# Kernel tuning notes

Hardware: AMD Instinct MI355X
Metric: run time of the kernel (lower is better)

Reference implementation:

```python
import jax, jax.numpy as jnp
import numpy as np

SRC, B, SNT, E, C, V, EXT = 512, 16, 512, 512, 512, 12000, 500


def setup_inputs() -> dict:
    key = jax.random.key(0)
    ks = jax.random.split(key, 12)
    alignment_weight = jax.random.uniform(ks[0], (SRC, B, SNT), dtype=jnp.float32)
    arc_weight = jax.random.uniform(ks[1], (SRC, B, SRC), dtype=jnp.float32)
    rel_weight = jnp.zeros((1,), jnp.float32)
    concept_outs = jax.random.normal(ks[2], (SRC, B, E), dtype=jnp.float32)
    copy_seq = jax.random.randint(ks[3], (SNT, B, 2), 0, V + EXT)
    # pin the max so tot_ext = V + EXT is deterministic (torch uses copy_seq.max().item())
    copy_seq = copy_seq.at[0, 0, 0].set(V + EXT - 1)
    target = jax.random.randint(ks[4], (SRC, B), 0, V)
    target_rel = jnp.zeros((1,), jnp.int64 if jax.config.read('jax_enable_x64') else jnp.int32)
    std = 0.02
    W_transfer = jax.random.normal(ks[5], (C, E), jnp.float32) * std
    b_transfer = jnp.zeros((C,), jnp.float32)
    W_gen = jax.random.normal(ks[6], (V, C), jnp.float32) * std
    b_gen = jnp.zeros((V,), jnp.float32)
    W_div = jax.random.normal(ks[7], (3, C), jnp.float32) * std
    b_div = jnp.zeros((3,), jnp.float32)
    return dict(alignment_weight=alignment_weight, arc_weight=arc_weight,
                rel_weight=rel_weight, concept_outs=concept_outs,
                copy_seq=copy_seq, target=target, target_rel=target_rel,
                bsz=B, src_len=SRC,
                W_transfer=W_transfer, b_transfer=b_transfer,
                W_gen=W_gen, b_gen=b_gen, W_div=W_div, b_div=b_div)


def reference(alignment_weight, arc_weight, rel_weight, concept_outs, copy_seq,
              target, target_rel, bsz, src_len,
              W_transfer, b_transfer, W_gen, b_gen, W_div, b_div):
    # work=True inference path of ArcConceptDecoder (joint_rel=False, separate_rel=False)
    snt_len = alignment_weight.shape[-1]
    copy_seq = copy_seq[:snt_len]                       # [snt, B, 2]
    h = jnp.tanh(concept_outs @ W_transfer.T + b_transfer)  # [src, B, C]
    gates = jax.nn.softmax(h @ W_div.T + b_div, axis=-1)     # [src, B, 3]
    gen_gate = gates[..., 0:1]
    map_gate = gates[..., 1:2]
    copy_gate = gates[..., 2:3]
    copy_gate2 = jnp.concatenate([copy_gate, map_gate], axis=-1)  # [src, B, 2]
    probs = gen_gate * jax.nn.softmax(h @ W_gen.T + b_gen, axis=-1)  # [src, B, V]
    vocab = probs.shape[-1]
    tot_ext = vocab + EXT
    probs = jnp.concatenate(
        [probs, jnp.zeros(probs.shape[:-1] + (tot_ext - vocab,), probs.dtype)], axis=-1)
    # index: copy_seq.transpose(0,1).view(1,B,-1).expand(src,-1,-1)
    index = jnp.transpose(copy_seq, (1, 0, 2)).reshape(1, probs.shape[1], -1)  # [1, B, snt*2]
    index = jnp.broadcast_to(index, (probs.shape[0],) + index.shape[1:])       # [src, B, snt*2]
    copy_probs = (copy_gate2[:, :, None, :] * alignment_weight[..., None])
    copy_probs = copy_probs.reshape(probs.shape[0], probs.shape[1], -1)        # [src, B, snt*2]
    # scatter_add along last dim
    S, Bv = probs.shape[0], probs.shape[1]
    flat_probs = probs.reshape(S * Bv, tot_ext)
    flat_idx = index.reshape(S * Bv, -1)
    flat_cp = copy_probs.reshape(S * Bv, -1)
    rows = jnp.arange(S * Bv)[:, None]
    flat_probs = flat_probs.at[rows, flat_idx].add(flat_cp)
    probs = flat_probs.reshape(S, Bv, tot_ext)
    ll = jnp.log(probs + 1e-12)
    arc_ll = jnp.log(arc_weight + 1e-12)
    return ll, arc_ll
```

## Files before the change

kernel.cpp:

```cpp
#include <hip/hip_runtime.h>
#include <hip/hip_bf16.h>

#define SRCL 512
#define BSZ  16
#define SNTL 512
#define CDIM 512
#define KDIM 512
#define VOC  12000
#define EXTN 500
#define MROWS (SRCL*BSZ)
#define TOTV (VOC+EXTN)
#define NPAD 12032
#define LL_SIZE ((size_t)MROWS * TOTV)

typedef __attribute__((ext_vector_type(8))) short bf16x8;
typedef __attribute__((ext_vector_type(4))) float f32x4;

__device__ __forceinline__ unsigned short f2bf(float x) {
  union { __hip_bfloat16 b; unsigned short u; } c;
  c.b = __float2bfloat16(x);
  return c.u;
}
__device__ __forceinline__ float bflo(unsigned int u) { return __uint_as_float(u << 16); }
__device__ __forceinline__ float bfhi(unsigned int u) { return __uint_as_float(u & 0xffff0000u); }

__device__ __forceinline__ void gload16(const void* g, void* l) {
  __builtin_amdgcn_global_load_lds(
      (const __attribute__((address_space(1))) unsigned int*)g,
      (__attribute__((address_space(3))) unsigned int*)l, 16, 0, 0);
}

__device__ __forceinline__ float wred_max(float v) {
  for (int o = 32; o; o >>= 1) v = fmaxf(v, __shfl_down(v, o, 64));
  return v;
}
__device__ __forceinline__ float wred_sum(float v) {
  for (int o = 32; o; o >>= 1) v += __shfl_down(v, o, 64);
  return v;
}

__global__ void cvt_kernel(const float* __restrict__ co, const float* __restrict__ wt,
                           const float* __restrict__ wg,
                           unsigned short* __restrict__ cob,
                           unsigned short* __restrict__ wtb,
                           unsigned short* __restrict__ wgb) {
  const int stride = gridDim.x * blockDim.x;
  const int t0 = blockIdx.x * blockDim.x + threadIdx.x;
  for (int i = t0; i < MROWS*KDIM/4; i += stride) {
    const float4 v = ((const float4*)co)[i];
    ushort4 o; o.x = f2bf(v.x); o.y = f2bf(v.y); o.z = f2bf(v.z); o.w = f2bf(v.w);
    ((ushort4*)cob)[i] = o;
  }
  for (int i = t0; i < CDIM*KDIM/4; i += stride) {
    const float4 v = ((const float4*)wt)[i];
    ushort4 o; o.x = f2bf(v.x); o.y = f2bf(v.y); o.z = f2bf(v.z); o.w = f2bf(v.w);
    ((ushort4*)wtb)[i] = o;
  }
  for (int i = t0; i < NPAD*KDIM/4; i += stride) {
    float4 v = make_float4(0.f, 0.f, 0.f, 0.f);
    if (i < VOC*KDIM/4) v = ((const float4*)wg)[i];
    ushort4 o; o.x = f2bf(v.x); o.y = f2bf(v.y); o.z = f2bf(v.z); o.w = f2bf(v.w);
    ((ushort4*)wgb)[i] = o;
  }
}

template<int EPI>
__launch_bounds__(256)
__global__ void gemm_bt(const short* __restrict__ A, const short* __restrict__ Bm,
                        const float* __restrict__ bias, void* __restrict__ outp) {
  __shared__ short As[128*32];
  __shared__ short Bs[128*32];
  const int tid  = threadIdx.x;
  const int wave = tid >> 6;
  const int lane = tid & 63;
  const int m0 = blockIdx.y * 128;
  const int n0 = blockIdx.x * 128;

  const int lrow = lane >> 2;
  const int lkof = (lane & 3) * 8;
  const size_t aG0 = (size_t)(m0 + wave*32 + lrow) * KDIM + lkof;
  const size_t aG1 = aG0 + (size_t)16 * KDIM;
  const size_t bG0 = (size_t)(n0 + wave*32 + lrow) * KDIM + lkof;
  const size_t bG1 = bG0 + (size_t)16 * KDIM;
  short* lA0 = As + wave*1024;  short* lA1 = lA0 + 512;
  short* lB0 = Bs + wave*1024;  short* lB1 = lB0 + 512;

  const int wm = wave & 1, wn = wave >> 1;
  const int quad = lane >> 4, r16 = lane & 15;
  const int aoff = (wm*64 + r16)*32 + quad*8;
  const int boff = (wn*64 + r16)*32 + quad*8;

  f32x4 acc[4][4];
#pragma unroll
  for (int i = 0; i < 4; ++i)
#pragma unroll
    for (int j = 0; j < 4; ++j) acc[i][j] = (f32x4){0.f,0.f,0.f,0.f};

  for (int kt = 0; kt < KDIM/32; ++kt) {
    const int kof = kt * 32;
    __syncthreads();
    gload16(A  + aG0 + kof, lA0);
    gload16(A  + aG1 + kof, lA1);
    gload16(Bm + bG0 + kof, lB0);
    gload16(Bm + bG1 + kof, lB1);
    __syncthreads();
    bf16x8 af[4], bf[4];
#pragma unroll
    for (int i = 0; i < 4; ++i) {
      af[i] = *(const bf16x8*)(As + aoff + i*512);
      bf[i] = *(const bf16x8*)(Bs + boff + i*512);
    }
#pragma unroll
    for (int mi = 0; mi < 4; ++mi)
#pragma unroll
      for (int ni = 0; ni < 4; ++ni)
        acc[mi][ni] = __builtin_amdgcn_mfma_f32_16x16x32_bf16(af[mi], bf[ni], acc[mi][ni], 0, 0, 0);
  }

#pragma unroll
  for (int mi = 0; mi < 4; ++mi) {
#pragma unroll
    for (int ni = 0; ni < 4; ++ni) {
#pragma unroll
      for (int r = 0; r < 4; ++r) {
        const int row = m0 + wm*64 + mi*16 + quad*4 + r;
        const int col = n0 + wn*64 + ni*16 + r16;
        float v = acc[mi][ni][r];
        if constexpr (EPI == 0) {
          v = tanhf(v + bias[col]);
          ((unsigned short*)outp)[(size_t)row * CDIM + col] = f2bf(v);
        } else if constexpr (EPI == 1) {
          v += (col < VOC) ? bias[col] : 0.f;
          ((float*)outp)[(size_t)row * TOTV + col] = v;
        } else {
          v += (col < VOC) ? bias[col] : 0.f;
          ((unsigned short*)outp)[(size_t)row * NPAD + col] = f2bf(v);
        }
      }
    }
  }
}

__launch_bounds__(256)
__global__ void gates_kernel(const __hip_bfloat16* __restrict__ h,
                             const float* __restrict__ Wd, const float* __restrict__ bd,
                             float* __restrict__ gates) {
  __shared__ float scr[12];
  const int m = blockIdx.x;
  float d0 = 0.f, d1 = 0.f, d2 = 0.f;
  for (int c = threadIdx.x; c < CDIM; c += 256) {
    const float hv = __bfloat162float(h[(size_t)m*CDIM + c]);
    d0 += hv * Wd[c];
    d1 += hv * Wd[CDIM + c];
    d2 += hv * Wd[2*CDIM + c];
  }
  d0 = wred_sum(d0); d1 = wred_sum(d1); d2 = wred_sum(d2);
  const int w = threadIdx.x >> 6;
  if ((threadIdx.x & 63) == 0) { scr[w*3] = d0; scr[w*3+1] = d1; scr[w*3+2] = d2; }
  __syncthreads();
  if (threadIdx.x == 0) {
    float g0 = bd[0], g1 = bd[1], g2 = bd[2];
    for (int i = 0; i < 4; ++i) { g0 += scr[i*3]; g1 += scr[i*3+1]; g2 += scr[i*3+2]; }
    const float mx = fmaxf(g0, fmaxf(g1, g2));
    const float e0 = __expf(g0-mx), e1 = __expf(g1-mx), e2 = __expf(g2-mx);
    const float inv = 1.f / (e0 + e1 + e2);
    gates[m*3+0] = e0*inv; gates[m*3+1] = e1*inv; gates[m*3+2] = e2*inv;
  }
}

template<int BF16L>
__launch_bounds__(1024)
__global__ void finalize_kernel(const void* __restrict__ lg, float* __restrict__ out,
                                const float* __restrict__ gates,
                                const int* __restrict__ copy_seq,
                                const float* __restrict__ align) {
  __shared__ __align__(16) float p[TOTV];
  __shared__ float scr[16];
  const int m = blockIdx.x;
  const int b = m & 15;
  const int tid = threadIdx.x;
  float* row = out + (size_t)m * TOTV;

  float mx = -1e30f;
  if constexpr (BF16L) {
    const uint4* rowv = (const uint4*)((const unsigned short*)lg + (size_t)m * NPAD);
    for (int i = tid; i < VOC/8; i += 1024) {
      const uint4 q = rowv[i];
      const float v0 = bflo(q.x), v1 = bfhi(q.x), v2 = bflo(q.y), v3 = bfhi(q.y);
      const float v4 = bflo(q.z), v5 = bfhi(q.z), v6 = bflo(q.w), v7 = bfhi(q.w);
      const int base = i*8;
      p[base+0]=v0; p[base+1]=v1; p[base+2]=v2; p[base+3]=v3;
      p[base+4]=v4; p[base+5]=v5; p[base+6]=v6; p[base+7]=v7;
      mx = fmaxf(mx, fmaxf(fmaxf(fmaxf(v0,v1),fmaxf(v2,v3)), fmaxf(fmaxf(v4,v5),fmaxf(v6,v7))));
    }
  } else {
    const float4* rowv = (const float4*)row;
    for (int i = tid; i < VOC/4; i += 1024) {
      const float4 v = rowv[i];
      ((float4*)p)[i] = v;
      mx = fmaxf(mx, fmaxf(fmaxf(v.x, v.y), fmaxf(v.z, v.w)));
    }
  }
  for (int i = VOC + tid; i < TOTV; i += 1024) p[i] = 0.f;

  mx = wred_max(mx);
  if ((tid & 63) == 0) scr[tid >> 6] = mx;
  __syncthreads();
  mx = scr[0];
#pragma unroll
  for (int i = 1; i < 16; ++i) mx = fmaxf(mx, scr[i]);
  __syncthreads();

  float sm = 0.f;
  for (int i = tid; i < VOC; i += 1024) {
    const float e = __expf(p[i] - mx);
    p[i] = e;
    sm += e;
  }
  sm = wred_sum(sm);
  if ((tid & 63) == 0) scr[tid >> 6] = sm;
  __syncthreads();
  sm = scr[0];
#pragma unroll
  for (int i = 1; i < 16; ++i) sm += scr[i];

  const float gen  = gates[m*3 + 0];
  const float mapg = gates[m*3 + 1];
  const float cpg  = gates[m*3 + 2];
  const float scale = gen / sm;
  const float inv   = sm / gen;
  const float cw = cpg * inv, mw = mapg * inv;

  if (tid < SNTL) {
    const float aw = align[(size_t)m * SNTL + tid];
    const int2 cs = *(const int2*)&copy_seq[(tid*BSZ + b)*2];
    atomicAdd(&p[cs.x], cw * aw);
    atomicAdd(&p[cs.y], mw * aw);
  }
  __syncthreads();

  for (int i = tid; i < TOTV/4; i += 1024) {
    const float4 v = ((const float4*)p)[i];
    float4 r;
    r.x = __logf(fmaf(v.x, scale, 1e-12f));
    r.y = __logf(fmaf(v.y, scale, 1e-12f));
    r.z = __logf(fmaf(v.z, scale, 1e-12f));
    r.w = __logf(fmaf(v.w, scale, 1e-12f));
    ((float4*)row)[i] = r;
  }
}

__global__ void arc_kernel(const float4* __restrict__ arc, float4* __restrict__ out) {
  const int i = blockIdx.x * blockDim.x + threadIdx.x;
  if (i < (SRCL*BSZ*SRCL)/4) {
    const float4 v = arc[i];
    float4 r;
    r.x = __logf(v.x + 1e-12f);
    r.y = __logf(v.y + 1e-12f);
    r.z = __logf(v.z + 1e-12f);
    r.w = __logf(v.w + 1e-12f);
    out[i] = r;
  }
}

extern "C" void kernel_launch(void* const* d_in, const int* in_sizes, int n_in,
                              void* d_out, int out_size, void* d_ws, size_t ws_size,
                              hipStream_t stream) {
  (void)in_sizes; (void)n_in; (void)out_size;
  const float* align   = (const float*)d_in[0];
  const float* arc     = (const float*)d_in[1];
  const float* concept = (const float*)d_in[3];
  const int*   cseq    = (const int*)d_in[4];
  const float* Wt = (const float*)d_in[9];
  const float* bt = (const float*)d_in[10];
  const float* Wg = (const float*)d_in[11];
  const float* bg = (const float*)d_in[12];
  const float* Wd = (const float*)d_in[13];
  const float* bd = (const float*)d_in[14];
  float* out = (float*)d_out;

  unsigned short* cob = (unsigned short*)d_ws;
  unsigned short* wtb = cob + (size_t)MROWS*KDIM;
  unsigned short* wgb = wtb + (size_t)CDIM*KDIM;
  unsigned short* hb  = wgb + (size_t)NPAD*KDIM;
  float* gates = (float*)(hb + (size_t)MROWS*KDIM);
  unsigned short* logitsb = (unsigned short*)(gates + (size_t)MROWS*3);
  const size_t need = (size_t)((char*)(logitsb + (size_t)MROWS*NPAD) - (char*)d_ws);
  const bool use_bf16_logits = (ws_size >= need);

  cvt_kernel<<<2048, 256, 0, stream>>>(concept, Wt, Wg, cob, wtb, wgb);
  gemm_bt<0><<<dim3(CDIM/128, MROWS/128), 256, 0, stream>>>(
      (const short*)cob, (const short*)wtb, bt, (void*)hb);
  gates_kernel<<<MROWS, 256, 0, stream>>>((const __hip_bfloat16*)hb, Wd, bd, gates);
  if (use_bf16_logits) {
    gemm_bt<2><<<dim3(NPAD/128, MROWS/128), 256, 0, stream>>>(
        (const short*)hb, (const short*)wgb, bg, (void*)logitsb);
    finalize_kernel<1><<<MROWS, 1024, 0, stream>>>(logitsb, out, gates, cseq, align);
  } else {
    gemm_bt<1><<<dim3(NPAD/128, MROWS/128), 256, 0, stream>>>(
        (const short*)hb, (const short*)wgb, bg, (void*)out);
    finalize_kernel<0><<<MROWS, 1024, 0, stream>>>(out, out, gates, cseq, align);
  }
  arc_kernel<<<4096, 256, 0, stream>>>((const float4*)arc, (float4*)(out + LL_SIZE));
}
```

Baseline: 801.4 us.

## Deepen GEMM K-tile with XOR-swizzled LDS, remap blocks, fuse gates into finalize

The GEMM now stages 64-wide K tiles with an XOR swizzle on LDS columns, which halves the number of barrier pairs and is meant to avoid LDS bank conflicts. Workgroup IDs are remapped in strides of 8, likely to spread neighbouring tiles across XCDs and improve L2 locality. The separate gates kernel is removed and the 3-way gate softmax is computed at the start of finalize_kernel, which saves a launch and a global round trip. In exchange the GEMM uses more LDS per block, and finalize gains an extra barrier and dot-product work.

Measured after the change: 823.5 us. +2.8%, slower.

```diff
diff --git a/kernel.cpp b/kernel.cpp
--- a/kernel.cpp
+++ b/kernel.cpp
@@ -68,27 +68,32 @@
 __launch_bounds__(256)
 __global__ void gemm_bt(const short* __restrict__ A, const short* __restrict__ Bm,
                         const float* __restrict__ bias, void* __restrict__ outp) {
-  __shared__ short As[128*32];
-  __shared__ short Bs[128*32];
+  __shared__ short As[128*64];
+  __shared__ short Bs[128*64];
   const int tid  = threadIdx.x;
   const int wave = tid >> 6;
   const int lane = tid & 63;
-  const int m0 = blockIdx.y * 128;
-  const int n0 = blockIdx.x * 128;
-
-  const int lrow = lane >> 2;
-  const int lkof = (lane & 3) * 8;
-  const size_t aG0 = (size_t)(m0 + wave*32 + lrow) * KDIM + lkof;
-  const size_t aG1 = aG0 + (size_t)16 * KDIM;
-  const size_t bG0 = (size_t)(n0 + wave*32 + lrow) * KDIM + lkof;
-  const size_t bG1 = bG0 + (size_t)16 * KDIM;
-  short* lA0 = As + wave*1024;  short* lA1 = lA0 + 512;
-  short* lB0 = Bs + wave*1024;  short* lB1 = lB0 + 512;
+
+  const int nwg = gridDim.x * gridDim.y;
+  int bid = blockIdx.y * gridDim.x + blockIdx.x;
+  bid = (bid & 7) * (nwg >> 3) + (bid >> 3);
+  const int bx = bid % gridDim.x;
+  const int by = bid / gridDim.x;
+  const int m0 = by * 128;
+  const int n0 = bx * 128;
+
+  const int srow = lane >> 3;
+  const int ssk  = ((lane & 7) ^ srow) * 8;
+  const size_t aBase = (size_t)(m0 + wave*32 + srow) * KDIM + ssk;
+  const size_t bBase = (size_t)(n0 + wave*32 + srow) * KDIM + ssk;
+  short* lA = As + wave*32*64;
+  short* lB = Bs + wave*32*64;
 
   const int wm = wave & 1, wn = wave >> 1;
   const int quad = lane >> 4, r16 = lane & 15;
-  const int aoff = (wm*64 + r16)*32 + quad*8;
-  const int boff = (wn*64 + r16)*32 + quad*8;
+  const int rsw  = r16 & 7;
+  const int aoffb = (wm*64 + r16) * 64;
+  const int boffb = (wn*64 + r16) * 64;
 
   f32x4 acc[4][4];
 #pragma unroll
@@ -96,25 +101,30 @@
 #pragma unroll
     for (int j = 0; j < 4; ++j) acc[i][j] = (f32x4){0.f,0.f,0.f,0.f};
 
-  for (int kt = 0; kt < KDIM/32; ++kt) {
-    const int kof = kt * 32;
+  for (int kt = 0; kt < KDIM/64; ++kt) {
+    const size_t ko = (size_t)kt * 64;
     __syncthreads();
-    gload16(A  + aG0 + kof, lA0);
-    gload16(A  + aG1 + kof, lA1);
-    gload16(Bm + bG0 + kof, lB0);
-    gload16(Bm + bG1 + kof, lB1);
+#pragma unroll
+    for (int j = 0; j < 4; ++j) {
+      gload16(A  + aBase + ko + (size_t)j*8*KDIM, lA + j*512);
+      gload16(Bm + bBase + ko + (size_t)j*8*KDIM, lB + j*512);
+    }
     __syncthreads();
-    bf16x8 af[4], bf[4];
-#pragma unroll
-    for (int i = 0; i < 4; ++i) {
-      af[i] = *(const bf16x8*)(As + aoff + i*512);
-      bf[i] = *(const bf16x8*)(Bs + boff + i*512);
-    }
-#pragma unroll
-    for (int mi = 0; mi < 4; ++mi)
-#pragma unroll
-      for (int ni = 0; ni < 4; ++ni)
-        acc[mi][ni] = __builtin_amdgcn_mfma_f32_16x16x32_bf16(af[mi], bf[ni], acc[mi][ni], 0, 0, 0);
+#pragma unroll
+    for (int ks = 0; ks < 2; ++ks) {
+      const int kc = ((ks*4 + quad) ^ rsw) * 8;
+      bf16x8 af[4], bf[4];
+#pragma unroll
+      for (int i = 0; i < 4; ++i) {
+        af[i] = *(const bf16x8*)(As + aoffb + i*1024 + kc);
+        bf[i] = *(const bf16x8*)(Bs + boffb + i*1024 + kc);
+      }
+#pragma unroll
+      for (int mi = 0; mi < 4; ++mi)
+#pragma unroll
+        for (int ni = 0; ni < 4; ++ni)
+          acc[mi][ni] = __builtin_amdgcn_mfma_f32_16x16x32_bf16(af[mi], bf[ni], acc[mi][ni], 0, 0, 0);
+    }
   }
 
 #pragma unroll
@@ -141,57 +151,56 @@
   }
 }
 
-__launch_bounds__(256)
-__global__ void gates_kernel(const __hip_bfloat16* __restrict__ h,
-                             const float* __restrict__ Wd, const float* __restrict__ bd,
-                             float* __restrict__ gates) {
-  __shared__ float scr[12];
-  const int m = blockIdx.x;
-  float d0 = 0.f, d1 = 0.f, d2 = 0.f;
-  for (int c = threadIdx.x; c < CDIM; c += 256) {
-    const float hv = __bfloat162float(h[(size_t)m*CDIM + c]);
-    d0 += hv * Wd[c];
-    d1 += hv * Wd[CDIM + c];
-    d2 += hv * Wd[2*CDIM + c];
-  }
-  d0 = wred_sum(d0); d1 = wred_sum(d1); d2 = wred_sum(d2);
-  const int w = threadIdx.x >> 6;
-  if ((threadIdx.x & 63) == 0) { scr[w*3] = d0; scr[w*3+1] = d1; scr[w*3+2] = d2; }
-  __syncthreads();
-  if (threadIdx.x == 0) {
-    float g0 = bd[0], g1 = bd[1], g2 = bd[2];
-    for (int i = 0; i < 4; ++i) { g0 += scr[i*3]; g1 += scr[i*3+1]; g2 += scr[i*3+2]; }
-    const float mx = fmaxf(g0, fmaxf(g1, g2));
-    const float e0 = __expf(g0-mx), e1 = __expf(g1-mx), e2 = __expf(g2-mx);
-    const float inv = 1.f / (e0 + e1 + e2);
-    gates[m*3+0] = e0*inv; gates[m*3+1] = e1*inv; gates[m*3+2] = e2*inv;
-  }
-}
-
 template<int BF16L>
 __launch_bounds__(1024)
 __global__ void finalize_kernel(const void* __restrict__ lg, float* __restrict__ out,
-                                const float* __restrict__ gates,
+                                const __hip_bfloat16* __restrict__ hmat,
+                                const float* __restrict__ Wd, const float* __restrict__ bd,
                                 const int* __restrict__ copy_seq,
                                 const float* __restrict__ align) {
   __shared__ __align__(16) float p[TOTV];
   __shared__ float scr[16];
+  __shared__ float gscr[24];
+  __shared__ float gv[3];
   const int m = blockIdx.x;
   const int b = m & 15;
   const int tid = threadIdx.x;
   float* row = out + (size_t)m * TOTV;
+
+  {
+    float d0 = 0.f, d1 = 0.f, d2 = 0.f;
+    if (tid < CDIM) {
+      const float hv = __bfloat162float(hmat[(size_t)m*CDIM + tid]);
+      d0 = hv * Wd[tid];
+      d1 = hv * Wd[CDIM + tid];
+      d2 = hv * Wd[2*CDIM + tid];
+    }
+    d0 = wred_sum(d0); d1 = wred_sum(d1); d2 = wred_sum(d2);
+    const int w = tid >> 6;
+    if ((tid & 63) == 0 && w < 8) { gscr[w*3] = d0; gscr[w*3+1] = d1; gscr[w*3+2] = d2; }
+  }
+  __syncthreads();
+  if (tid == 0) {
+    float g0 = bd[0], g1 = bd[1], g2 = bd[2];
+    for (int i = 0; i < 8; ++i) { g0 += gscr[i*3]; g1 += gscr[i*3+1]; g2 += gscr[i*3+2]; }
+    const float mg = fmaxf(g0, fmaxf(g1, g2));
+    const float e0 = __expf(g0-mg), e1 = __expf(g1-mg), e2 = __expf(g2-mg);
+    const float inv3 = 1.f / (e0 + e1 + e2);
+    gv[0] = e0*inv3; gv[1] = e1*inv3; gv[2] = e2*inv3;
+  }
 
   float mx = -1e30f;
   if constexpr (BF16L) {
     const uint4* rowv = (const uint4*)((const unsigned short*)lg + (size_t)m * NPAD);
     for (int i = tid; i < VOC/8; i += 1024) {
       const uint4 q = rowv[i];
-      const float v0 = bflo(q.x), v1 = bfhi(q.x), v2 = bflo(q.y), v3 = bfhi(q.y);
-      const float v4 = bflo(q.z), v5 = bfhi(q.z), v6 = bflo(q.w), v7 = bfhi(q.w);
-      const int base = i*8;
-      p[base+0]=v0; p[base+1]=v1; p[base+2]=v2; p[base+3]=v3;
-      p[base+4]=v4; p[base+5]=v5; p[base+6]=v6; p[base+7]=v7;
-      mx = fmaxf(mx, fmaxf(fmaxf(fmaxf(v0,v1),fmaxf(v2,v3)), fmaxf(fmaxf(v4,v5),fmaxf(v6,v7))));
+      float4 lo, hi;
+      lo.x = bflo(q.x); lo.y = bfhi(q.x); lo.z = bflo(q.y); lo.w = bfhi(q.y);
+      hi.x = bflo(q.z); hi.y = bfhi(q.z); hi.z = bflo(q.w); hi.w = bfhi(q.w);
+      ((float4*)p)[i*2]   = lo;
+      ((float4*)p)[i*2+1] = hi;
+      mx = fmaxf(mx, fmaxf(fmaxf(fmaxf(lo.x,lo.y),fmaxf(lo.z,lo.w)),
+                           fmaxf(fmaxf(hi.x,hi.y),fmaxf(hi.z,hi.w))));
     }
   } else {
     const float4* rowv = (const float4*)row;
@@ -224,9 +233,9 @@
 #pragma unroll
   for (int i = 1; i < 16; ++i) sm += scr[i];
 
-  const float gen  = gates[m*3 + 0];
-  const float mapg = gates[m*3 + 1];
-  const float cpg  = gates[m*3 + 2];
+  const float gen  = gv[0];
+  const float mapg = gv[1];
+  const float cpg  = gv[2];
   const float scale = gen / sm;
   const float inv   = sm / gen;
   const float cw = cpg * inv, mw = mapg * inv;
@@ -283,23 +292,23 @@
   unsigned short* wtb = cob + (size_t)MROWS*KDIM;
   unsigned short* wgb = wtb + (size_t)CDIM*KDIM;
   unsigned short* hb  = wgb + (size_t)NPAD*KDIM;
-  float* gates = (float*)(hb + (size_t)MROWS*KDIM);
-  unsigned short* logitsb = (unsigned short*)(gates + (size_t)MROWS*3);
+  unsigned short* logitsb = hb + (size_t)MROWS*KDIM;
   const size_t need = (size_t)((char*)(logitsb + (size_t)MROWS*NPAD) - (char*)d_ws);
   const bool use_bf16_logits = (ws_size >= need);
 
   cvt_kernel<<<2048, 256, 0, stream>>>(concept, Wt, Wg, cob, wtb, wgb);
   gemm_bt<0><<<dim3(CDIM/128, MROWS/128), 256, 0, stream>>>(
       (const short*)cob, (const short*)wtb, bt, (void*)hb);
-  gates_kernel<<<MROWS, 256, 0, stream>>>((const __hip_bfloat16*)hb, Wd, bd, gates);
   if (use_bf16_logits) {
     gemm_bt<2><<<dim3(NPAD/128, MROWS/128), 256, 0, stream>>>(
         (const short*)hb, (const short*)wgb, bg, (void*)logitsb);
-    finalize_kernel<1><<<MROWS, 1024, 0, stream>>>(logitsb, out, gates, cseq, align);
+    finalize_kernel<1><<<MROWS, 1024, 0, stream>>>(
+        logitsb, out, (const __hip_bfloat16*)hb, Wd, bd, cseq, align);
   } else {
     gemm_bt<1><<<dim3(NPAD/128, MROWS/128), 256, 0, stream>>>(
         (const short*)hb, (const short*)wgb, bg, (void*)out);
-    finalize_kernel<0><<<MROWS, 1024, 0, stream>>>(out, out, gates, cseq, align);
+    finalize_kernel<0><<<MROWS, 1024, 0, stream>>>(
+        out, out, (const __hip_bfloat16*)hb, Wd, bd, cseq, align);
   }
   arc_kernel<<<4096, 256, 0, stream>>>((const float4*)arc, (float4*)(out + LL_SIZE));
 }
```
